# Optimization experiments

Hardware: AMD Instinct MI355X
Metric: run time of the kernel (lower is better)

Reference implementation:

```python
import jax, jax.numpy as jnp
import numpy as np

B, T = 256, 1024
V, E, H = 27, 64, 128


def setup_inputs() -> dict:
    key = jax.random.key(0)
    ks = jax.random.split(key, 8)
    return {
        "x": jax.random.randint(ks[0], (B, T), 0, V, dtype=jnp.int32),
        "emb": jax.random.normal(ks[1], (V, E), dtype=jnp.float32) * 0.02,
        "wx0": jax.random.normal(ks[2], (E, 4 * H), dtype=jnp.float32) * 0.01,
        "wh0": jax.random.normal(ks[3], (H, 4 * H), dtype=jnp.float32) * 0.01,
        "b0": jnp.zeros((4 * H,), dtype=jnp.float32),
        "wx1": jax.random.normal(ks[4], (H, 4 * H), dtype=jnp.float32) * 0.01,
        "wh1": jax.random.normal(ks[5], (H, 4 * H), dtype=jnp.float32) * 0.01,
        "b1": jnp.zeros((4 * H,), dtype=jnp.float32),
        "why": jax.random.normal(ks[6], (H, V), dtype=jnp.float32),
        "by": jnp.zeros((V,), dtype=jnp.float32),
    }


def _cell(xt, h_prev, c_prev, wx, wh, b):
    # gates: [B, 4H]; chunk order matches torch .chunk(4): f, i, g, o
    gates = xt @ wx + h_prev @ wh + b
    ft, it, gt, ot = jnp.split(gates, 4, axis=1)
    c_t = jax.nn.sigmoid(ft) * c_prev + jax.nn.sigmoid(it) * jnp.tanh(gt)
    h_t = jnp.tanh(c_t) * jax.nn.sigmoid(ot)
    return h_t, c_t


def reference(x, emb, wx0, wh0, b0, wx1, wh1, b1, why, by):
    Bx = x.shape[0]
    xe = emb[x]                       # [B, T, E]
    xe = jnp.swapaxes(xe, 0, 1)       # [T, B, E] for scan over time
    h0 = jnp.zeros((Bx, H), jnp.float32)
    c0 = jnp.zeros((Bx, H), jnp.float32)
    h1 = jnp.zeros((Bx, H), jnp.float32)
    c1 = jnp.zeros((Bx, H), jnp.float32)

    def step(carry, xt):
        h0, c0, h1, c1 = carry
        h0, c0 = _cell(xt, h0, c0, wx0, wh0, b0)   # layer 0
        h1, c1 = _cell(h0, h1, c1, wx1, wh1, b1)   # layer 1 (dropout off in eval)
        yt = h1 @ why + by                         # [B, V]
        return (h0, c0, h1, c1), yt

    _, ys = jax.lax.scan(step, (h0, c0, h1, c1), xe)  # ys: [T, B, V]
    return jnp.swapaxes(ys, 0, 1)                     # [B, T, V]
```

## Files before the change

### kernel.cpp

```cpp
#include <hip/hip_runtime.h>


#define B_  256
#define T_  1024
#define V_  27
#define E_  64
#define H_  128
#define G4  512
#define TPITCH 528

typedef float v2f __attribute__((ext_vector_type(2)));

__device__ __forceinline__ v2f mkv2(float a, float b) { v2f r; r.x = a; r.y = b; return r; }

template <int CTRL>
__device__ __forceinline__ float dppmov(float v) {
    return __int_as_float(__builtin_amdgcn_update_dpp(
               0, __float_as_int(v), CTRL, 0xF, 0xF, true));
}
__device__ __forceinline__ float qsum(float v) {
    v += dppmov<0xB1>(v);
    v += dppmov<0x4E>(v);
    return v;
}
__device__ __forceinline__ float tanh_fast(float y) {
    const float t = expf(2.f * y);
    return fmaf(-2.f, __builtin_amdgcn_rcpf(t + 1.f), 1.f);
}

#define REPEAT16(M) M(0) M(1) M(2) M(3) M(4) M(5) M(6) M(7) \
                    M(8) M(9) M(10) M(11) M(12) M(13) M(14) M(15)

#define DECLW(K) v2f wf##K, wi##K, wg##K, wo##K;
#define LOADW(K) { const float* r0 = wmat + (size_t)(kb + 2*(K)) * G4; \
                   wf##K = mkv2(r0[p],          r0[G4 + p]); \
                   wi##K = mkv2(r0[H_ + p],     r0[G4 + H_ + p]); \
                   wg##K = mkv2(r0[2*H_ + p],   r0[G4 + 2*H_ + p]); \
                   wo##K = mkv2(r0[3*H_ + p],   r0[G4 + 3*H_ + p]); }
#define FMAP(K, HA, HB) { const v2f h2 = mkv2(HA, HB); \
    sf2 = __builtin_elementwise_fma(h2, wf##K, sf2); \
    si2 = __builtin_elementwise_fma(h2, wi##K, si2); \
    sg2 = __builtin_elementwise_fma(h2, wg##K, sg2); \
    so2 = __builtin_elementwise_fma(h2, wo##K, so2); }

#define FMABODY \
    v2f sf2 = mkv2(0.f, 0.f), si2 = sf2, sg2 = sf2, so2 = sf2; \
    FMAP(0,  v0.x, v0.y) FMAP(1,  v0.z, v0.w) \
    FMAP(2,  v1.x, v1.y) FMAP(3,  v1.z, v1.w) \
    FMAP(4,  v2.x, v2.y) FMAP(5,  v2.z, v2.w) \
    FMAP(6,  v3.x, v3.y) FMAP(7,  v3.z, v3.w) \
    FMAP(8,  v4.x, v4.y) FMAP(9,  v4.z, v4.w) \
    FMAP(10, v5.x, v5.y) FMAP(11, v5.z, v5.w) \
    FMAP(12, v6.x, v6.y) FMAP(13, v6.z, v6.w) \
    FMAP(14, v7.x, v7.y) FMAP(15, v7.z, v7.w)

__global__ __launch_bounds__(G4)
void build_table0(const float* __restrict__ emb,
                  const float* __restrict__ wx0,
                  const float* __restrict__ b0,
                  float* __restrict__ table0)
{
    const int v = blockIdx.x;
    const int j = threadIdx.x;
    __shared__ float e[E_];
    if (j < E_) e[j] = emb[v * E_ + j];
    __syncthreads();
    float s = b0[j];
#pragma unroll 8
    for (int k = 0; k < E_; ++k) s += e[k] * wx0[k * G4 + j];
    const int r = j & (H_ - 1), gate = j >> 7;
    table0[v * TPITCH + gate * 132 + r] = s;
}

__global__ __launch_bounds__(512, 2)
void lstm_l0_chunk(const int* __restrict__ x,
                   const float* __restrict__ table0,
                   const float* __restrict__ wh0,
                   float* __restrict__ h0st, float* __restrict__ c0st,
                   float* __restrict__ h0buf,
                   int t0, int TC)
{
    const int j = threadIdx.x;
    const int p = j >> 2;
    const int e = j & 3;
    const int b = blockIdx.x;
    const int kb = 32 * e;

    __shared__ __align__(16) float hP[2][4][36];
    __shared__ __align__(16) float tabS[V_ * TPITCH];

    const float* wmat = wh0;
    REPEAT16(DECLW)
    REPEAT16(LOADW)
    for (int i = j; i < V_ * TPITCH; i += 512) tabS[i] = table0[i];
    if (j < H_) hP[0][j >> 5][j & 31] = h0st[b * H_ + j];
    float c = c0st[b * H_ + p];
    float hh = 0.f;
    __syncthreads();

    const int* xb = x + (size_t)b * T_ + t0;
    float* hob = h0buf + (size_t)b * TC * H_;
    const float A = (e == 2) ? 2.f : 1.f;

    int idx = xb[0];
    for (int t = 0; t < TC; ++t) {
        const int idxn = (t + 1 < TC) ? xb[t + 1] : 0;
        const float tv = tabS[idx * TPITCH + e * 132 + p];

        const float4* hb4 = reinterpret_cast<const float4*>(&hP[t & 1][e][0]);
        const float4 v0 = hb4[0], v1 = hb4[1], v2 = hb4[2], v3 = hb4[3],
                     v4 = hb4[4], v5 = hb4[5], v6 = hb4[6], v7 = hb4[7];
        FMABODY
        const float sf = qsum(sf2.x + sf2.y);
        const float si = qsum(si2.x + si2.y);
        const float sg = qsum(sg2.x + sg2.y);
        const float so = qsum(so2.x + so2.y);

        float val = (e == 0) ? sf : (e == 1) ? si : (e == 2) ? sg : so;
        val += tv;
        const float tz  = expf(A * val);
        const float act = fmaf(-A, __builtin_amdgcn_rcpf(tz + 1.f), 1.f);

        const float iv = dppmov<0x39>(act);
        const float gv = dppmov<0x4E>(act);
        const float ov = dppmov<0x93>(act);
        c  = fmaf(act, c, iv * gv);
        hh = tanh_fast(c) * ov;

        if (e == 0) {
            hP[(t + 1) & 1][p >> 5][p & 31] = hh;
            hob[(size_t)t * H_ + p] = hh;
        }
        idx = idxn;
        __syncthreads();
    }
    if (e == 0) { h0st[b * H_ + p] = hh; c0st[b * H_ + p] = c; }
}

__global__ __launch_bounds__(G4, 2)
void gemm_xg1(const float* __restrict__ h0buf,
              const float* __restrict__ wx1,
              const float* __restrict__ b1,
              float* __restrict__ xg1)
{
    const int j  = threadIdx.x;
    const size_t m0 = (size_t)blockIdx.x * 64;
    const int c  = j & 127;
    const int rg = j >> 7;

    __shared__ __align__(16) float aT[64 * 132];

#pragma unroll
    for (int i = 0; i < 4; ++i) {
        const int e  = i * G4 + j;
        const int r  = e >> 5;
        const int k4 = e & 31;
        const float4 v = *reinterpret_cast<const float4*>(&h0buf[(m0 + r) * H_ + k4 * 4]);
        *reinterpret_cast<float4*>(&aT[r * 132 + k4 * 4]) = v;
    }
    __syncthreads();

    float acc[4][16];
#pragma unroll
    for (int cc = 0; cc < 4; ++cc)
#pragma unroll
        for (int rr = 0; rr < 16; ++rr) acc[cc][rr] = 0.f;

    for (int k4 = 0; k4 < 32; ++k4) {
        float bv[4][4];
#pragma unroll
        for (int kk = 0; kk < 4; ++kk)
#pragma unroll
            for (int cc = 0; cc < 4; ++cc)
                bv[kk][cc] = wx1[(size_t)(k4 * 4 + kk) * G4 + cc * 128 + c];
#pragma unroll
        for (int rr = 0; rr < 16; ++rr) {
            const float4 av = *reinterpret_cast<const float4*>(&aT[(rg * 16 + rr) * 132 + k4 * 4]);
#pragma unroll
            for (int cc = 0; cc < 4; ++cc) {
                acc[cc][rr] = fmaf(av.x, bv[0][cc], acc[cc][rr]);
                acc[cc][rr] = fmaf(av.y, bv[1][cc], acc[cc][rr]);
                acc[cc][rr] = fmaf(av.z, bv[2][cc], acc[cc][rr]);
                acc[cc][rr] = fmaf(av.w, bv[3][cc], acc[cc][rr]);
            }
        }
    }

    float b1v[4];
#pragma unroll
    for (int cc = 0; cc < 4; ++cc) b1v[cc] = b1[cc * 128 + c];
#pragma unroll
    for (int rr = 0; rr < 16; ++rr) {
        const size_t row = m0 + rg * 16 + rr;
#pragma unroll
        for (int cc = 0; cc < 4; ++cc)
            xg1[row * G4 + cc * 128 + c] = acc[cc][rr] + b1v[cc];
    }
}

__global__ __launch_bounds__(512, 2)
void lstm_l1_chunk(const float* __restrict__ xg1,
                   const float* __restrict__ wh1,
                   float* __restrict__ h1st, float* __restrict__ c1st,
                   float* __restrict__ h1buf,
                   int TC)
{
    const int j = threadIdx.x;
    const int p = j >> 2;
    const int e = j & 3;
    const int b = blockIdx.x;
    const int kb = 32 * e;

    __shared__ __align__(16) float hP[2][4][36];

    const float* wmat = wh1;
    REPEAT16(DECLW)
    REPEAT16(LOADW)
    if (j < H_) hP[0][j >> 5][j & 31] = h1st[b * H_ + j];
    float c = c1st[b * H_ + p];
    float hh = 0.f;
    __syncthreads();

    const float* xgb = xg1 + (size_t)b * TC * G4;
    float* hob = h1buf + (size_t)b * TC * H_;
    const float A = (e == 2) ? 2.f : 1.f;
    const int xcol = e * H_ + p;

    float xv = xgb[xcol];
    for (int t = 0; t < TC; ++t) {
        const float xvn = (t + 1 < TC) ? xgb[(size_t)(t + 1) * G4 + xcol] : 0.f;

        const float4* hb4 = reinterpret_cast<const float4*>(&hP[t & 1][e][0]);
        const float4 v0 = hb4[0], v1 = hb4[1], v2 = hb4[2], v3 = hb4[3],
                     v4 = hb4[4], v5 = hb4[5], v6 = hb4[6], v7 = hb4[7];
        FMABODY
        const float sf = qsum(sf2.x + sf2.y);
        const float si = qsum(si2.x + si2.y);
        const float sg = qsum(sg2.x + sg2.y);
        const float so = qsum(so2.x + so2.y);

        float val = (e == 0) ? sf : (e == 1) ? si : (e == 2) ? sg : so;
        val += xv;
        const float tz  = expf(A * val);
        const float act = fmaf(-A, __builtin_amdgcn_rcpf(tz + 1.f), 1.f);

        const float iv = dppmov<0x39>(act);
        const float gv = dppmov<0x4E>(act);
        const float ov = dppmov<0x93>(act);
        c  = fmaf(act, c, iv * gv);
        hh = tanh_fast(c) * ov;

        if (e == 0) {
            hP[(t + 1) & 1][p >> 5][p & 31] = hh;
            hob[(size_t)t * H_ + p] = hh;
        }
        xv = xvn;
        __syncthreads();
    }
    if (e == 0) { h1st[b * H_ + p] = hh; c1st[b * H_ + p] = c; }
}

__global__ __launch_bounds__(256)
void proj_y(const float* __restrict__ h1buf,
            const float* __restrict__ why,
            const float* __restrict__ by,
            float* __restrict__ out,
            int t0, int TC)
{
    const int tid = threadIdx.x;
    const int b   = blockIdx.x;

    __shared__ __align__(16) float whyS[V_][H_];
    __shared__ float byS[V_];
    __shared__ float yS[256][29];

    for (int e = tid; e < V_ * H_; e += 256) {
        const int v = e / H_, k = e - v * H_;
        whyS[v][k] = why[k * V_ + v];
    }
    if (tid < V_) byS[tid] = by[tid];
    __syncthreads();

    const float* hb  = h1buf + (size_t)b * TC * H_;
    float* outb      = out + ((size_t)b * T_ + t0) * V_;

    for (int tt0 = 0; tt0 < TC; tt0 += 256) {
        const int tt = tt0 + tid;
        if (tt < TC) {
            float acc[V_];
#pragma unroll
            for (int v = 0; v < V_; ++v) acc[v] = byS[v];
            const float4* hr = reinterpret_cast<const float4*>(hb + (size_t)tt * H_);
#pragma unroll 4
            for (int k4 = 0; k4 < 32; ++k4) {
                const float4 hv = hr[k4];
#pragma unroll
                for (int v = 0; v < V_; ++v) {
                    const float4 wv = *reinterpret_cast<const float4*>(&whyS[v][k4 * 4]);
                    acc[v] = fmaf(hv.x, wv.x,
                             fmaf(hv.y, wv.y,
                             fmaf(hv.z, wv.z,
                             fmaf(hv.w, wv.w, acc[v]))));
                }
            }
#pragma unroll
            for (int v = 0; v < V_; ++v) yS[tid][v] = acc[v];
        }
        __syncthreads();
        const int nrow = (TC - tt0 < 256) ? (TC - tt0) : 256;
        const int n = nrow * V_;
        float* od = outb + (size_t)tt0 * V_;
        for (int i = tid; i < n; i += 256) {
            const int r = i / V_, v = i - r * V_;
            od[i] = yS[r][v];
        }
        __syncthreads();
    }
}

__global__ __launch_bounds__(G4, 1)
void lstm_persist(const int* __restrict__ x,
                  const float* __restrict__ table0,
                  const float* __restrict__ wh0,
                  const float* __restrict__ wx1,
                  const float* __restrict__ wh1,
                  const float* __restrict__ b1,
                  const float* __restrict__ why,
                  const float* __restrict__ by,
                  float* __restrict__ out)
{
    const int j  = threadIdx.x;
    const int bb = blockIdx.x * 2;

    __shared__ float h0s[2][H_], c0s[2][H_], h1s[2][H_], c1s[2][H_];
    __shared__ float hcat[2][2 * H_];
    __shared__ float g0s[2][G4], g1s[2][G4];
    __shared__ float whyS[H_ * V_];
    __shared__ float b1S[G4];
    __shared__ float byS[V_];
    __shared__ float pb[2][V_][8];

    for (int i = j; i < H_ * V_; i += G4) whyS[i] = why[i];
    b1S[j] = b1[j];
    if (j < V_) byS[j] = by[j];
    if (j < H_) {
        h0s[0][j] = 0.f; h0s[1][j] = 0.f; c0s[0][j] = 0.f; c0s[1][j] = 0.f;
        h1s[0][j] = 0.f; h1s[1][j] = 0.f; c1s[0][j] = 0.f; c1s[1][j] = 0.f;
    }
    __syncthreads();

    const int* xA = x + (size_t)(bb + 0) * T_;
    const int* xB = x + (size_t)(bb + 1) * T_;
    float* outA = out + (size_t)(bb + 0) * T_ * V_;
    float* outB = out + (size_t)(bb + 1) * T_ * V_;

    const int tix = (j >> 7) * 132 + (j & (H_ - 1));

    for (int t = 0; t < T_; ++t) {
        const int ia = xA[t];
        const int ib = xB[t];
        float aA = table0[ia * TPITCH + tix];
        float aB = table0[ib * TPITCH + tix];
#pragma unroll 8
        for (int k = 0; k < H_; ++k) {
            const float w = wh0[k * G4 + j];
            aA += h0s[0][k] * w;
            aB += h0s[1][k] * w;
        }
        g0s[0][j] = aA; g0s[1][j] = aB;
        __syncthreads();

        if (j < 2 * H_) {
            const int gi = j >> 7, r = j & (H_ - 1);
            const float f  = 1.f / (1.f + expf(-g0s[gi][r]));
            const float i_ = 1.f / (1.f + expf(-g0s[gi][H_ + r]));
            const float g  = tanhf(g0s[gi][2 * H_ + r]);
            const float o  = 1.f / (1.f + expf(-g0s[gi][3 * H_ + r]));
            const float c  = f * c0s[gi][r] + i_ * g;
            c0s[gi][r] = c;
            const float h = tanhf(c) * o;
            h0s[gi][r] = h;
            hcat[gi][r] = h;
            hcat[gi][H_ + r] = h1s[gi][r];
        }
        __syncthreads();

        float bA = b1S[j];
        float bB = bA;
#pragma unroll 8
        for (int k = 0; k < H_; ++k) {
            const float w = wx1[k * G4 + j];
            bA += hcat[0][k] * w;
            bB += hcat[1][k] * w;
        }
#pragma unroll 8
        for (int k = 0; k < H_; ++k) {
            const float w = wh1[k * G4 + j];
            bA += hcat[0][H_ + k] * w;
            bB += hcat[1][H_ + k] * w;
        }
        g1s[0][j] = bA; g1s[1][j] = bB;
        __syncthreads();

        if (j < 2 * H_) {
            const int gi = j >> 7, r = j & (H_ - 1);
            const float f  = 1.f / (1.f + expf(-g1s[gi][r]));
            const float i_ = 1.f / (1.f + expf(-g1s[gi][H_ + r]));
            const float g  = tanhf(g1s[gi][2 * H_ + r]);
            const float o  = 1.f / (1.f + expf(-g1s[gi][3 * H_ + r]));
            const float c  = f * c1s[gi][r] + i_ * g;
            c1s[gi][r] = c;
            h1s[gi][r] = tanhf(c) * o;
        }
        __syncthreads();

        if (j < 2 * V_ * 8) {
            int q = j;
            const int gi = (q >= V_ * 8) ? 1 : 0;
            q -= gi * V_ * 8;
            const int v = q >> 3, kk = q & 7;
            float pv = 0.f;
#pragma unroll
            for (int k = kk * 16; k < kk * 16 + 16; ++k)
                pv += h1s[gi][k] * whyS[k * V_ + v];
            pb[gi][v][kk] = pv;
        }
        __syncthreads();

        if (j < 2 * V_) {
            const int gi = (j >= V_) ? 1 : 0;
            const int v  = j - gi * V_;
            float s = byS[v];
#pragma unroll
            for (int q = 0; q < 8; ++q) s += pb[gi][v][q];
            (gi ? outB : outA)[t * V_ + v] = s;
        }
        __syncthreads();
    }
}

extern "C" void kernel_launch(void* const* d_in, const int* in_sizes, int n_in,
                              void* d_out, int out_size, void* d_ws, size_t ws_size,
                              hipStream_t stream)
{
    const int*   x   = (const int*)  d_in[0];
    const float* emb = (const float*)d_in[1];
    const float* wx0 = (const float*)d_in[2];
    const float* wh0 = (const float*)d_in[3];
    const float* b0  = (const float*)d_in[4];
    const float* wx1 = (const float*)d_in[5];
    const float* wh1 = (const float*)d_in[6];
    const float* b1  = (const float*)d_in[7];
    const float* why = (const float*)d_in[8];
    const float* by  = (const float*)d_in[9];
    float* out = (float*)d_out;
    float* wsf = (float*)d_ws;

    const size_t tabF   = (size_t)V_ * TPITCH;
    const size_t stateF = (size_t)4 * B_ * H_;

    int TC = 0;
    for (int tc = T_; tc >= 32; tc >>= 1) {
        const size_t need = (tabF + stateF + (size_t)B_ * tc * (H_ + G4 + H_)) * 4;
        if (need <= ws_size) { TC = tc; break; }
    }

    float* table0 = wsf;
    build_table0<<<dim3(V_), dim3(G4), 0, stream>>>(emb, wx0, b0, table0);

    if (TC == 0) {
        lstm_persist<<<dim3(B_ / 2), dim3(G4), 0, stream>>>(
            x, table0, wh0, wx1, wh1, b1, why, by, out);
        return;
    }

    float* h0st   = wsf + tabF;
    float* c0st   = h0st + (size_t)B_ * H_;
    float* h1st   = c0st + (size_t)B_ * H_;
    float* c1st   = h1st + (size_t)B_ * H_;
    float* h0buf  = c1st + (size_t)B_ * H_;
    float* xg1buf = h0buf + (size_t)B_ * TC * H_;
    float* h1buf  = xg1buf + (size_t)B_ * TC * G4;

    (void)hipMemsetAsync(h0st, 0, stateF * sizeof(float), stream);

    const int NC = T_ / TC;
    for (int c = 0; c < NC; ++c) {
        const int t0 = c * TC;
        lstm_l0_chunk<<<dim3(B_), dim3(512), 0, stream>>>(
            x, table0, wh0, h0st, c0st, h0buf, t0, TC);
        gemm_xg1<<<dim3(4 * TC), dim3(G4), 0, stream>>>(
            h0buf, wx1, b1, xg1buf);
        lstm_l1_chunk<<<dim3(B_), dim3(512), 0, stream>>>(
            xg1buf, wh1, h1st, c1st, h1buf, TC);
        proj_y<<<dim3(B_), dim3(256), 0, stream>>>(
            h1buf, why, by, out, t0, TC);
    }
}
```

Before: 2.004 ms.

## Overlap layer-1 recurrence of one chunk with layer-0 of the next

Moves the two per-layer recurrent loops into device functions and adds a fused kernel. Its first half of blocks runs layer 1 on chunk c while its second half runs layer 0 on chunk c+1, giving a software pipeline across time chunks. The chunk size is capped at 256 so there are several chunks to pipeline, with prologue and epilogue launches for the first layer-0 and last layer-1 chunks. The aim is to fill the GPU with two latency-bound recurrences at once instead of running them serially. In exchange there are more launches and chunk boundaries, and every fused block statically reserves the large embedding-table LDS buffer, which limits residency.

```diff
diff --git a/kernel.cpp b/kernel.cpp
--- a/kernel.cpp
+++ b/kernel.cpp
@@ -54,6 +54,124 @@
     FMAP(12, v6.x, v6.y) FMAP(13, v6.z, v6.w) \
     FMAP(14, v7.x, v7.y) FMAP(15, v7.z, v7.w)
 
+__device__ __forceinline__ void l0_body(
+    const int j, const int b,
+    const int* __restrict__ x, const float* __restrict__ table0,
+    const float* __restrict__ wh0,
+    float* __restrict__ h0st, float* __restrict__ c0st,
+    float* __restrict__ h0buf, int t0, int TC,
+    float (*hP)[4][36], float* tabS)
+{
+    const int p = j >> 2;
+    const int e = j & 3;
+    const int kb = 32 * e;
+
+    const float* wmat = wh0;
+    REPEAT16(DECLW)
+    REPEAT16(LOADW)
+    for (int i = j; i < V_ * TPITCH; i += 512) tabS[i] = table0[i];
+    if (j < H_) hP[0][j >> 5][j & 31] = h0st[b * H_ + j];
+    float c = c0st[b * H_ + p];
+    float hh = 0.f;
+    __syncthreads();
+
+    const int* xb = x + (size_t)b * T_ + t0;
+    float* hob = h0buf + (size_t)b * TC * H_;
+    const float A = (e == 2) ? 2.f : 1.f;
+
+    int idx = xb[0];
+    for (int t = 0; t < TC; ++t) {
+        const int idxn = (t + 1 < TC) ? xb[t + 1] : 0;
+        const float tv = tabS[idx * TPITCH + e * 132 + p];
+
+        const float4* hb4 = reinterpret_cast<const float4*>(&hP[t & 1][e][0]);
+        const float4 v0 = hb4[0], v1 = hb4[1], v2 = hb4[2], v3 = hb4[3],
+                     v4 = hb4[4], v5 = hb4[5], v6 = hb4[6], v7 = hb4[7];
+        FMABODY
+        const float sf = qsum(sf2.x + sf2.y);
+        const float si = qsum(si2.x + si2.y);
+        const float sg = qsum(sg2.x + sg2.y);
+        const float so = qsum(so2.x + so2.y);
+
+        float val = (e == 0) ? sf : (e == 1) ? si : (e == 2) ? sg : so;
+        val += tv;
+        const float tz  = expf(A * val);
+        const float act = fmaf(-A, __builtin_amdgcn_rcpf(tz + 1.f), 1.f);
+
+        const float iv = dppmov<0x39>(act);
+        const float gv = dppmov<0x4E>(act);
+        const float ov = dppmov<0x93>(act);
+        c  = fmaf(act, c, iv * gv);
+        hh = tanh_fast(c) * ov;
+
+        if (e == 0) {
+            hP[(t + 1) & 1][p >> 5][p & 31] = hh;
+            hob[(size_t)t * H_ + p] = hh;
+        }
+        idx = idxn;
+        __syncthreads();
+    }
+    if (e == 0) { h0st[b * H_ + p] = hh; c0st[b * H_ + p] = c; }
+}
+
+__device__ __forceinline__ void l1_body(
+    const int j, const int b,
+    const float* __restrict__ xg1, const float* __restrict__ wh1,
+    float* __restrict__ h1st, float* __restrict__ c1st,
+    float* __restrict__ h1buf, int TC,
+    float (*hP)[4][36])
+{
+    const int p = j >> 2;
+    const int e = j & 3;
+    const int kb = 32 * e;
+
+    const float* wmat = wh1;
+    REPEAT16(DECLW)
+    REPEAT16(LOADW)
+    if (j < H_) hP[0][j >> 5][j & 31] = h1st[b * H_ + j];
+    float c = c1st[b * H_ + p];
+    float hh = 0.f;
+    __syncthreads();
+
+    const float* xgb = xg1 + (size_t)b * TC * G4;
+    float* hob = h1buf + (size_t)b * TC * H_;
+    const float A = (e == 2) ? 2.f : 1.f;
+    const int xcol = e * H_ + p;
+
+    float xv = xgb[xcol];
+    for (int t = 0; t < TC; ++t) {
+        const float xvn = (t + 1 < TC) ? xgb[(size_t)(t + 1) * G4 + xcol] : 0.f;
+
+        const float4* hb4 = reinterpret_cast<const float4*>(&hP[t & 1][e][0]);
+        const float4 v0 = hb4[0], v1 = hb4[1], v2 = hb4[2], v3 = hb4[3],
+                     v4 = hb4[4], v5 = hb4[5], v6 = hb4[6], v7 = hb4[7];
+        FMABODY
+        const float sf = qsum(sf2.x + sf2.y);
+        const float si = qsum(si2.x + si2.y);
+        const float sg = qsum(sg2.x + sg2.y);
+        const float so = qsum(so2.x + so2.y);
+
+        float val = (e == 0) ? sf : (e == 1) ? si : (e == 2) ? sg : so;
+        val += xv;
+        const float tz  = expf(A * val);
+        const float act = fmaf(-A, __builtin_amdgcn_rcpf(tz + 1.f), 1.f);
+
+        const float iv = dppmov<0x39>(act);
+        const float gv = dppmov<0x4E>(act);
+        const float ov = dppmov<0x93>(act);
+        c  = fmaf(act, c, iv * gv);
+        hh = tanh_fast(c) * ov;
+
+        if (e == 0) {
+            hP[(t + 1) & 1][p >> 5][p & 31] = hh;
+            hob[(size_t)t * H_ + p] = hh;
+        }
+        xv = xvn;
+        __syncthreads();
+    }
+    if (e == 0) { h1st[b * H_ + p] = hh; c1st[b * H_ + p] = c; }
+}
+
 __global__ __launch_bounds__(G4)
 void build_table0(const float* __restrict__ emb,
                   const float* __restrict__ wx0,
@@ -80,61 +198,44 @@
                    float* __restrict__ h0buf,
                    int t0, int TC)
 {
-    const int j = threadIdx.x;
-    const int p = j >> 2;
-    const int e = j & 3;
-    const int b = blockIdx.x;
-    const int kb = 32 * e;
-
     __shared__ __align__(16) float hP[2][4][36];
     __shared__ __align__(16) float tabS[V_ * TPITCH];
-
-    const float* wmat = wh0;
-    REPEAT16(DECLW)
-    REPEAT16(LOADW)
-    for (int i = j; i < V_ * TPITCH; i += 512) tabS[i] = table0[i];
-    if (j < H_) hP[0][j >> 5][j & 31] = h0st[b * H_ + j];
-    float c = c0st[b * H_ + p];
-    float hh = 0.f;
-    __syncthreads();
-
-    const int* xb = x + (size_t)b * T_ + t0;
-    float* hob = h0buf + (size_t)b * TC * H_;
-    const float A = (e == 2) ? 2.f : 1.f;
-
-    int idx = xb[0];
-    for (int t = 0; t < TC; ++t) {
-        const int idxn = (t + 1 < TC) ? xb[t + 1] : 0;
-        const float tv = tabS[idx * TPITCH + e * 132 + p];
-
-        const float4* hb4 = reinterpret_cast<const float4*>(&hP[t & 1][e][0]);
-        const float4 v0 = hb4[0], v1 = hb4[1], v2 = hb4[2], v3 = hb4[3],
-                     v4 = hb4[4], v5 = hb4[5], v6 = hb4[6], v7 = hb4[7];
-        FMABODY
-        const float sf = qsum(sf2.x + sf2.y);
-        const float si = qsum(si2.x + si2.y);
-        const float sg = qsum(sg2.x + sg2.y);
-        const float so = qsum(so2.x + so2.y);
-
-        float val = (e == 0) ? sf : (e == 1) ? si : (e == 2) ? sg : so;
-        val += tv;
-        const float tz  = expf(A * val);
-        const float act = fmaf(-A, __builtin_amdgcn_rcpf(tz + 1.f), 1.f);
-
-        const float iv = dppmov<0x39>(act);
-        const float gv = dppmov<0x4E>(act);
-        const float ov = dppmov<0x93>(act);
-        c  = fmaf(act, c, iv * gv);
-        hh = tanh_fast(c) * ov;
-
-        if (e == 0) {
-            hP[(t + 1) & 1][p >> 5][p & 31] = hh;
-            hob[(size_t)t * H_ + p] = hh;
-        }
-        idx = idxn;
-        __syncthreads();
-    }
-    if (e == 0) { h0st[b * H_ + p] = hh; c0st[b * H_ + p] = c; }
+    l0_body(threadIdx.x, blockIdx.x, x, table0, wh0, h0st, c0st, h0buf, t0, TC,
+            hP, tabS);
+}
+
+__global__ __launch_bounds__(512, 2)
+void lstm_l1_chunk(const float* __restrict__ xg1,
+                   const float* __restrict__ wh1,
+                   float* __restrict__ h1st, float* __restrict__ c1st,
+                   float* __restrict__ h1buf,
+                   int TC)
+{
+    __shared__ __align__(16) float hP[2][4][36];
+    l1_body(threadIdx.x, blockIdx.x, xg1, wh1, h1st, c1st, h1buf, TC, hP);
+}
+
+__global__ __launch_bounds__(512, 2)
+void lstm_fused(const int* __restrict__ x,
+                const float* __restrict__ table0,
+                const float* __restrict__ wh0,
+                const float* __restrict__ xg1,
+                const float* __restrict__ wh1,
+                float* __restrict__ h0st, float* __restrict__ c0st,
+                float* __restrict__ h0buf,
+                float* __restrict__ h1st, float* __restrict__ c1st,
+                float* __restrict__ h1buf,
+                int t0_l0, int TC)
+{
+    __shared__ __align__(16) float hP[2][4][36];
+    __shared__ __align__(16) float tabS[V_ * TPITCH];
+    const int bid = blockIdx.x;
+    if (bid < B_) {
+        l1_body(threadIdx.x, bid, xg1, wh1, h1st, c1st, h1buf, TC, hP);
+    } else {
+        l0_body(threadIdx.x, bid - B_, x, table0, wh0, h0st, c0st, h0buf,
+                t0_l0, TC, hP, tabS);
+    }
 }
 
 __global__ __launch_bounds__(G4, 2)
@@ -196,68 +297,6 @@
         for (int cc = 0; cc < 4; ++cc)
             xg1[row * G4 + cc * 128 + c] = acc[cc][rr] + b1v[cc];
     }
-}
-
-__global__ __launch_bounds__(512, 2)
-void lstm_l1_chunk(const float* __restrict__ xg1,
-                   const float* __restrict__ wh1,
-                   float* __restrict__ h1st, float* __restrict__ c1st,
-                   float* __restrict__ h1buf,
-                   int TC)
-{
-    const int j = threadIdx.x;
-    const int p = j >> 2;
-    const int e = j & 3;
-    const int b = blockIdx.x;
-    const int kb = 32 * e;
-
-    __shared__ __align__(16) float hP[2][4][36];
-
-    const float* wmat = wh1;
-    REPEAT16(DECLW)
-    REPEAT16(LOADW)
-    if (j < H_) hP[0][j >> 5][j & 31] = h1st[b * H_ + j];
-    float c = c1st[b * H_ + p];
-    float hh = 0.f;
-    __syncthreads();
-
-    const float* xgb = xg1 + (size_t)b * TC * G4;
-    float* hob = h1buf + (size_t)b * TC * H_;
-    const float A = (e == 2) ? 2.f : 1.f;
-    const int xcol = e * H_ + p;
-
-    float xv = xgb[xcol];
-    for (int t = 0; t < TC; ++t) {
-        const float xvn = (t + 1 < TC) ? xgb[(size_t)(t + 1) * G4 + xcol] : 0.f;
-
-        const float4* hb4 = reinterpret_cast<const float4*>(&hP[t & 1][e][0]);
-        const float4 v0 = hb4[0], v1 = hb4[1], v2 = hb4[2], v3 = hb4[3],
-                     v4 = hb4[4], v5 = hb4[5], v6 = hb4[6], v7 = hb4[7];
-        FMABODY
-        const float sf = qsum(sf2.x + sf2.y);
-        const float si = qsum(si2.x + si2.y);
-        const float sg = qsum(sg2.x + sg2.y);
-        const float so = qsum(so2.x + so2.y);
-
-        float val = (e == 0) ? sf : (e == 1) ? si : (e == 2) ? sg : so;
-        val += xv;
-        const float tz  = expf(A * val);
-        const float act = fmaf(-A, __builtin_amdgcn_rcpf(tz + 1.f), 1.f);
-
-        const float iv = dppmov<0x39>(act);
-        const float gv = dppmov<0x4E>(act);
-        const float ov = dppmov<0x93>(act);
-        c  = fmaf(act, c, iv * gv);
-        hh = tanh_fast(c) * ov;
-
-        if (e == 0) {
-            hP[(t + 1) & 1][p >> 5][p & 31] = hh;
-            hob[(size_t)t * H_ + p] = hh;
-        }
-        xv = xvn;
-        __syncthreads();
-    }
-    if (e == 0) { h1st[b * H_ + p] = hh; c1st[b * H_ + p] = c; }
 }
 
 __global__ __launch_bounds__(256)
@@ -460,7 +499,7 @@
     const size_t stateF = (size_t)4 * B_ * H_;
 
     int TC = 0;
-    for (int tc = T_; tc >= 32; tc >>= 1) {
+    for (int tc = 256; tc >= 32; tc >>= 1) {
         const size_t need = (tabF + stateF + (size_t)B_ * tc * (H_ + G4 + H_)) * 4;
         if (need <= ws_size) { TC = tc; break; }
     }
@@ -485,15 +524,23 @@
     (void)hipMemsetAsync(h0st, 0, stateF * sizeof(float), stream);
 
     const int NC = T_ / TC;
-    for (int c = 0; c < NC; ++c) {
-        const int t0 = c * TC;
-        lstm_l0_chunk<<<dim3(B_), dim3(512), 0, stream>>>(
-            x, table0, wh0, h0st, c0st, h0buf, t0, TC);
-        gemm_xg1<<<dim3(4 * TC), dim3(G4), 0, stream>>>(
-            h0buf, wx1, b1, xg1buf);
-        lstm_l1_chunk<<<dim3(B_), dim3(512), 0, stream>>>(
-            xg1buf, wh1, h1st, c1st, h1buf, TC);
+
+    lstm_l0_chunk<<<dim3(B_), dim3(512), 0, stream>>>(
+        x, table0, wh0, h0st, c0st, h0buf, 0, TC);
+    gemm_xg1<<<dim3(4 * TC), dim3(G4), 0, stream>>>(h0buf, wx1, b1, xg1buf);
+
+    for (int c = 0; c < NC - 1; ++c) {
+        lstm_fused<<<dim3(2 * B_), dim3(512), 0, stream>>>(
+            x, table0, wh0, xg1buf, wh1,
+            h0st, c0st, h0buf, h1st, c1st, h1buf,
+            (c + 1) * TC, TC);
+        gemm_xg1<<<dim3(4 * TC), dim3(G4), 0, stream>>>(h0buf, wx1, b1, xg1buf);
         proj_y<<<dim3(B_), dim3(256), 0, stream>>>(
-            h1buf, why, by, out, t0, TC);
-    }
-}
+            h1buf, why, by, out, c * TC, TC);
+    }
+
+    lstm_l1_chunk<<<dim3(B_), dim3(512), 0, stream>>>(
+        xg1buf, wh1, h1st, c1st, h1buf, TC);
+    proj_y<<<dim3(B_), dim3(256), 0, stream>>>(
+        h1buf, why, by, out, (NC - 1) * TC, TC);
+}
```

Result: no change. 2.004 ms (+0.0%).
